# Performance work log

Measured on AMD Instinct MI355X. Metric: run time of the kernel, lower is better.

Reference implementation:

```python
import jax, jax.numpy as jnp
import numpy as np

B, S, D = 32, 4096, 64        # batch, n_vec, n_dim
L = 13                        # n_link_all (chord links: 0, 1, 2, 4, ..., 2048)
NW = 13                       # n_W sparse-multiply rounds
HF, HV = 128, 128             # fnet / vnet hidden widths
NC = 2                        # n_class
VOCAB = 512
OFFSETS = [0] + [2 ** k for k in range(L - 1)]  # static python ints


def setup_inputs() -> dict:
    key = jax.random.key(0)
    ks = jax.random.split(key, 8)
    sn = lambda k, shape, sc: (jax.random.normal(k, shape, jnp.float32) * sc)
    return {
        "inputs": jax.random.randint(ks[0], (B, S), 0, VOCAB),
        "emb":  sn(ks[1], (VOCAB, D), 1.0),          # frozen embedding table
        "fW1":  sn(ks[2], (NW, D, HF), 0.1),         # stacked FNet layer-1 weights
        "fb1":  jnp.zeros((NW, HF), jnp.float32),
        "fW2":  sn(ks[3], (NW, HF, L), 0.1),         # stacked FNet layer-2 weights
        "fb2":  jnp.zeros((NW, L), jnp.float32),
        "vW1":  sn(ks[4], (D, HV), 0.1),
        "vb1":  jnp.zeros((HV,), jnp.float32),
        "vW2":  sn(ks[5], (HV, D), 0.1),
        "vb2":  jnp.zeros((D,), jnp.float32),
        "finW": sn(ks[6], (NC, S * D), 0.02),        # torch Linear weight (out, in)
        "finb": jnp.zeros((NC,), jnp.float32),
    }


def _gelu(x):
    return jax.nn.gelu(x, approximate=False)  # torch nn.GELU default (erf)


def reference(inputs, emb, fW1, fb1, fW2, fb2, vW1, vb1, vW2, vb2, finW, finb):
    X = emb[inputs]                                                  # (B,S,D)
    # all NW FNets at once: (NW,B,S,L)
    H = _gelu(jnp.einsum('bsd,kdh->kbsh', X, fW1) + fb1[:, None, None, :])
    Fs = jnp.einsum('kbsh,khl->kbsl', H, fW2) + fb2[:, None, None, :]
    # VNet
    V = _gelu(X @ vW1 + vb1) @ vW2 + vb2                             # (B,S,D)
    # chord sparse multiply rounds with residual:
    # Z[b,i,:] <- sum_l F[b,i,l] * Z[b,(i+off_l) mod S,:]  ;  Z += V
    Z = V
    for k in range(NW):
        Fk = Fs[k]                                                   # (B,S,L)
        Zn = Fk[..., 0][..., None] * Z                               # offset 0
        for l in range(1, L):
            Zn = Zn + Fk[..., l][..., None] * jnp.roll(Z, -OFFSETS[l], axis=1)
        Z = Zn + V
    # NOTE: original source computes logits from V (Z is overwritten); we
    # also return Z so the sparse-multiply loop stays live.
    out = V.reshape(B, S * D) @ finW.T + finb                        # (B,NC)
    return out, Z
```

## Files before the change

### kernel.cpp

```cpp
#include <hip/hip_runtime.h>
#include <hip/hip_bf16.h>
#include <hip/hip_fp16.h>
#include <math.h>

#define S_LEN   4096
#define B_SZ    32
#define D_DIM   64
#define L_LNK   13
#define NW_R    13
#define HF_W    128
#define HV_W    128
#define VOCAB_N 512
#define NC_N    2

#define STRIDE  512
#define NROW    8
#define MIRROR  256
#define BUFN    (S_LEN + MIRROR)

typedef float vf4 __attribute__((ext_vector_type(4)));

__device__ __forceinline__ float gelu_erf(float x) {
    return 0.5f * x * (1.0f + erff(x * 0.70710678118654752440f));
}

__device__ __forceinline__ uint2 pack4h(vf4 v) {
    __half2 a = __float22half2_rn(float2{v.x, v.y});
    __half2 b = __float22half2_rn(float2{v.z, v.w});
    uint2 r;
    r.x = *reinterpret_cast<unsigned int*>(&a);
    r.y = *reinterpret_cast<unsigned int*>(&b);
    return r;
}

__device__ __forceinline__ void fma_mix4_lo(vf4& a, unsigned cw, uint2 z) {
    float x = a.x, y = a.y, zz = a.z, w = a.w;
    asm("v_fma_mix_f32 %0, %4, %5, %0 op_sel:[0,0,0] op_sel_hi:[1,1,0]\n\t"
        "v_fma_mix_f32 %1, %4, %5, %1 op_sel:[0,1,0] op_sel_hi:[1,1,0]\n\t"
        "v_fma_mix_f32 %2, %4, %6, %2 op_sel:[0,0,0] op_sel_hi:[1,1,0]\n\t"
        "v_fma_mix_f32 %3, %4, %6, %3 op_sel:[0,1,0] op_sel_hi:[1,1,0]"
        : "+v"(x), "+v"(y), "+v"(zz), "+v"(w)
        : "v"(cw), "v"(z.x), "v"(z.y));
    a.x = x; a.y = y; a.z = zz; a.w = w;
}

__device__ __forceinline__ void fma_mix4_hi(vf4& a, unsigned cw, uint2 z) {
    float x = a.x, y = a.y, zz = a.z, w = a.w;
    asm("v_fma_mix_f32 %0, %4, %5, %0 op_sel:[1,0,0] op_sel_hi:[1,1,0]\n\t"
        "v_fma_mix_f32 %1, %4, %5, %1 op_sel:[1,1,0] op_sel_hi:[1,1,0]\n\t"
        "v_fma_mix_f32 %2, %4, %6, %2 op_sel:[1,0,0] op_sel_hi:[1,1,0]\n\t"
        "v_fma_mix_f32 %3, %4, %6, %3 op_sel:[1,1,0] op_sel_hi:[1,1,0]"
        : "+v"(x), "+v"(y), "+v"(zz), "+v"(w)
        : "v"(cw), "v"(z.x), "v"(z.y));
    a.x = x; a.y = y; a.z = zz; a.w = w;
}

__device__ __forceinline__ vf4 fma_mix4_init(unsigned cw, uint2 z, vf4 c) {
    float x, y, zz, w;
    asm("v_fma_mix_f32 %0, %4, %5, %7 op_sel:[0,0,0] op_sel_hi:[1,1,0]\n\t"
        "v_fma_mix_f32 %1, %4, %5, %8 op_sel:[0,1,0] op_sel_hi:[1,1,0]\n\t"
        "v_fma_mix_f32 %2, %4, %6, %9 op_sel:[0,0,0] op_sel_hi:[1,1,0]\n\t"
        "v_fma_mix_f32 %3, %4, %6, %10 op_sel:[0,1,0] op_sel_hi:[1,1,0]"
        : "=&v"(x), "=&v"(y), "=&v"(zz), "=&v"(w)
        : "v"(cw), "v"(z.x), "v"(z.y),
          "v"(c.x), "v"(c.y), "v"(c.z), "v"(c.w));
    vf4 r; r.x = x; r.y = y; r.z = zz; r.w = w;
    return r;
}

__global__ __launch_bounds__(128)
void tables_kernel(const float* __restrict__ emb,
                   const float* __restrict__ fW1, const float* __restrict__ fb1,
                   const float* __restrict__ fW2, const float* __restrict__ fb2,
                   const float* __restrict__ vW1, const float* __restrict__ vb1,
                   const float* __restrict__ vW2, const float* __restrict__ vb2,
                   __half* __restrict__ F_table, float* __restrict__ V_table) {
    __shared__ float s_emb[D_DIM];
    __shared__ float s_H[HF_W];
    const int blk = blockIdx.x;
    const int tid = threadIdx.x;

    if (blk < NW_R * VOCAB_N) {
        const int k = blk >> 9;
        const int t = blk & (VOCAB_N - 1);
        if (tid < D_DIM) s_emb[tid] = emb[t * D_DIM + tid];
        __syncthreads();
        float acc = fb1[k * HF_W + tid];
        const float* w = fW1 + (size_t)k * D_DIM * HF_W + tid;
        #pragma unroll 8
        for (int d = 0; d < D_DIM; ++d) acc += s_emb[d] * w[d * HF_W];
        s_H[tid] = gelu_erf(acc);
        __syncthreads();
        if (tid < 16) {
            float o = 0.0f;
            if (tid < L_LNK) {
                o = fb2[k * L_LNK + tid];
                const float* w2 = fW2 + (size_t)k * HF_W * L_LNK + tid;
                #pragma unroll 8
                for (int h = 0; h < HF_W; ++h) o += s_H[h] * w2[h * L_LNK];
            }
            F_table[((size_t)(k * VOCAB_N + t)) * 16 + tid] = __float2half_rn(o);
        }
    } else {
        const int t = blk - NW_R * VOCAB_N;
        if (tid < D_DIM) s_emb[tid] = emb[t * D_DIM + tid];
        __syncthreads();
        float acc = vb1[tid];
        const float* w = vW1 + tid;
        #pragma unroll 8
        for (int d = 0; d < D_DIM; ++d) acc += s_emb[d] * w[d * HV_W];
        s_H[tid] = gelu_erf(acc);
        __syncthreads();
        if (tid < D_DIM) {
            float o = vb2[tid];
            const float* w2 = vW2 + tid;
            #pragma unroll 8
            for (int h = 0; h < HV_W; ++h) o += s_H[h] * w2[h * D_DIM];
            V_table[t * D_DIM + tid] = o;
        }
    }
}

__global__ __launch_bounds__(512)
void logits_kernel(const int* __restrict__ tok,
                   const float* __restrict__ V_table,
                   const float* __restrict__ finW,
                   const float* __restrict__ finb,
                   float* __restrict__ out) {
    const int b = blockIdx.x >> 3;
    const int chunk = blockIdx.x & 7;
    const int tid = threadIdx.x;
    const int s = chunk * 512 + tid;
    const int t = tok[b * S_LEN + s];
    const float4* vp = (const float4*)V_table + t * 16;
    const float4* f0 = (const float4*)finW + s * 16;
    const float4* f1 = (const float4*)(finW + (size_t)S_LEN * D_DIM) + s * 16;
    float a0 = 0.0f, a1 = 0.0f;
    #pragma unroll
    for (int j = 0; j < 16; ++j) {
        float4 v = vp[j], x = f0[j], y = f1[j];
        a0 += v.x * x.x + v.y * x.y + v.z * x.z + v.w * x.w;
        a1 += v.x * y.x + v.y * y.y + v.z * y.z + v.w * y.w;
    }
    #pragma unroll
    for (int o = 32; o > 0; o >>= 1) {
        a0 += __shfl_down(a0, o, 64);
        a1 += __shfl_down(a1, o, 64);
    }
    __shared__ float sp[2][8];
    if ((tid & 63) == 0) { sp[0][tid >> 6] = a0; sp[1][tid >> 6] = a1; }
    __syncthreads();
    if (tid == 0) {
        float s0 = 0.0f, s1 = 0.0f;
        #pragma unroll
        for (int i = 0; i < 8; ++i) { s0 += sp[0][i]; s1 += sp[1][i]; }
        if (chunk == 0) { s0 += finb[0]; s1 += finb[1]; }
        atomicAdd(&out[b * NC_N + 0], s0);
        atomicAdd(&out[b * NC_N + 1], s1);
    }
}

__global__ __launch_bounds__(512, 4)
void chord_kernel(const int* __restrict__ tok,
                  const __half* __restrict__ F_table,
                  const float* __restrict__ V_table,
                  float* __restrict__ Zout) {
    __shared__ uint2 Zs[2][BUFN];
    const int b = blockIdx.y;
    const int ds = blockIdx.x;
    const int t = threadIdx.x;
    const vf4* V4 = (const vf4*)V_table;

    unsigned tokf[NROW];
    vf4 Vf[NROW];
    uint2 zp[NROW];
    #pragma unroll
    for (int j = 0; j < NROW; ++j) {
        const int r = t + STRIDE * j;
        const int tk = tok[b * S_LEN + r];
        tokf[j] = (unsigned)tk * 32u;
        vf4 v = V4[tk * 16 + ds];
        Vf[j] = v;
        uint2 p = pack4h(v);
        zp[j] = p;
        Zs[0][r] = p;
    }
    if (t < MIRROR) Zs[0][S_LEN + t] = zp[0];
    __syncthreads();

    int cur = 0;
    vf4 acc[NROW];
    #pragma unroll 1
    for (int k = 0; k < NW_R; ++k) {
        const char* Fk = (const char*)F_table + (size_t)k * (VOCAB_N * 32);
        const uint2* Zc = Zs[cur];
        #pragma unroll
        for (int j = 0; j < NROW; ++j) {
            const int r = t + STRIDE * j;
            const char* Fr = Fk + tokf[j];
            uint4 u0 = *(const uint4*)Fr;
            uint2 u1 = *(const uint2*)(Fr + 16);
            unsigned u2 = *(const unsigned*)(Fr + 24);
            vf4 a = fma_mix4_init(u0.x, zp[j], Vf[j]);
            fma_mix4_lo(a, u1.y, zp[(j + 1) & 7]);
            fma_mix4_hi(a, u1.y, zp[(j + 2) & 7]);
            fma_mix4_lo(a, u2,   zp[(j + 4) & 7]);
            fma_mix4_hi(a, u0.x, Zc[r + 1]);
            fma_mix4_lo(a, u0.y, Zc[r + 2]);
            fma_mix4_hi(a, u0.y, Zc[r + 4]);
            fma_mix4_lo(a, u0.z, Zc[r + 8]);
            fma_mix4_hi(a, u0.z, Zc[r + 16]);
            fma_mix4_lo(a, u0.w, Zc[r + 32]);
            fma_mix4_hi(a, u0.w, Zc[r + 64]);
            fma_mix4_lo(a, u1.x, Zc[r + 128]);
            fma_mix4_hi(a, u1.x, Zc[r + 256]);
            acc[j] = a;
        }
        if (k < NW_R - 1) {
            uint2* Zn = Zs[cur ^ 1];
            #pragma unroll
            for (int j = 0; j < NROW; ++j) {
                uint2 p = pack4h(acc[j]);
                zp[j] = p;
                Zn[t + STRIDE * j] = p;
            }
            if (t < MIRROR) Zn[S_LEN + t] = zp[0];
        }
        __syncthreads();
        cur ^= 1;
    }

    #pragma unroll
    for (int j = 0; j < NROW; ++j) {
        const int r = t + STRIDE * j;
        *(vf4*)(Zout + (((size_t)b * S_LEN + r) << 6) + ds * 4) = acc[j];
    }
}

extern "C" void kernel_launch(void* const* d_in, const int* in_sizes, int n_in,
                              void* d_out, int out_size, void* d_ws, size_t ws_size,
                              hipStream_t stream) {
    const int*   tok  = (const int*)d_in[0];
    const float* emb  = (const float*)d_in[1];
    const float* fW1  = (const float*)d_in[2];
    const float* fb1  = (const float*)d_in[3];
    const float* fW2  = (const float*)d_in[4];
    const float* fb2  = (const float*)d_in[5];
    const float* vW1  = (const float*)d_in[6];
    const float* vb1  = (const float*)d_in[7];
    const float* vW2  = (const float*)d_in[8];
    const float* vb2  = (const float*)d_in[9];
    const float* finW = (const float*)d_in[10];
    const float* finb = (const float*)d_in[11];

    float* out = (float*)d_out;
    float* Z   = out + B_SZ * NC_N;

    float*  V_table = (float*)d_ws;
    __half* F_table = (__half*)(V_table + VOCAB_N * D_DIM);

    hipMemsetAsync(out, 0, B_SZ * NC_N * sizeof(float), stream);
    tables_kernel<<<NW_R * VOCAB_N + VOCAB_N, 128, 0, stream>>>(
        emb, fW1, fb1, fW2, fb2, vW1, vb1, vW2, vb2, F_table, V_table);
    logits_kernel<<<B_SZ * NC_N * 4, 512, 0, stream>>>(tok, V_table, finW, finb, out);
    chord_kernel<<<dim3(16, B_SZ), 512, 0, stream>>>(tok, F_table, V_table, Z);
}
```

Before: 215.7 us.

## Double chord block size, keep V in half, parallelize FNet layer-2 reduction

The chord kernel now uses 1024 threads with 4 rows each instead of 512 threads with 8 rows. The offset-512 link moves from registers to shared memory, and the mirror region grows to 512 entries. V is kept as packed halves and fed as the addend of the initial mixed FMA, which cuts register pressure and is meant to raise latency hiding. In the tables kernel, the serial 13-thread layer-2 dot product becomes a per-thread partial product reduced by wave shuffles. The costs are one extra LDS read per row, V rounded to fp16 inside the accumulation, and a larger shared buffer.

```diff
diff --git a/kernel.cpp b/kernel.cpp
--- a/kernel.cpp
+++ b/kernel.cpp
@@ -13,9 +13,10 @@
 #define VOCAB_N 512
 #define NC_N    2
 
-#define STRIDE  512
-#define NROW    8
-#define MIRROR  256
+#define NT      1024
+#define STRIDE  1024
+#define NROW    4
+#define MIRROR  512
 #define BUFN    (S_LEN + MIRROR)
 
 typedef float vf4 __attribute__((ext_vector_type(4)));
@@ -55,15 +56,14 @@
     a.x = x; a.y = y; a.z = zz; a.w = w;
 }
 
-__device__ __forceinline__ vf4 fma_mix4_init(unsigned cw, uint2 z, vf4 c) {
+__device__ __forceinline__ vf4 fma_mix4_init_h(unsigned cw, uint2 z, uint2 v) {
     float x, y, zz, w;
-    asm("v_fma_mix_f32 %0, %4, %5, %7 op_sel:[0,0,0] op_sel_hi:[1,1,0]\n\t"
-        "v_fma_mix_f32 %1, %4, %5, %8 op_sel:[0,1,0] op_sel_hi:[1,1,0]\n\t"
-        "v_fma_mix_f32 %2, %4, %6, %9 op_sel:[0,0,0] op_sel_hi:[1,1,0]\n\t"
-        "v_fma_mix_f32 %3, %4, %6, %10 op_sel:[0,1,0] op_sel_hi:[1,1,0]"
+    asm("v_fma_mix_f32 %0, %4, %5, %7 op_sel:[0,0,0] op_sel_hi:[1,1,1]\n\t"
+        "v_fma_mix_f32 %1, %4, %5, %7 op_sel:[0,1,1] op_sel_hi:[1,1,1]\n\t"
+        "v_fma_mix_f32 %2, %4, %6, %8 op_sel:[0,0,0] op_sel_hi:[1,1,1]\n\t"
+        "v_fma_mix_f32 %3, %4, %6, %8 op_sel:[0,1,1] op_sel_hi:[1,1,1]"
         : "=&v"(x), "=&v"(y), "=&v"(zz), "=&v"(w)
-        : "v"(cw), "v"(z.x), "v"(z.y),
-          "v"(c.x), "v"(c.y), "v"(c.z), "v"(c.w));
+        : "v"(cw), "v"(z.x), "v"(z.y), "v"(v.x), "v"(v.y));
     vf4 r; r.x = x; r.y = y; r.z = zz; r.w = w;
     return r;
 }
@@ -77,6 +77,7 @@
                    __half* __restrict__ F_table, float* __restrict__ V_table) {
     __shared__ float s_emb[D_DIM];
     __shared__ float s_H[HF_W];
+    __shared__ float s_red[2][16];
     const int blk = blockIdx.x;
     const int tid = threadIdx.x;
 
@@ -89,16 +90,24 @@
         const float* w = fW1 + (size_t)k * D_DIM * HF_W + tid;
         #pragma unroll 8
         for (int d = 0; d < D_DIM; ++d) acc += s_emb[d] * w[d * HF_W];
-        s_H[tid] = gelu_erf(acc);
-        __syncthreads();
-        if (tid < 16) {
-            float o = 0.0f;
-            if (tid < L_LNK) {
-                o = fb2[k * L_LNK + tid];
-                const float* w2 = fW2 + (size_t)k * HF_W * L_LNK + tid;
-                #pragma unroll 8
-                for (int h = 0; h < HF_W; ++h) o += s_H[h] * w2[h * L_LNK];
-            }
+        const float hval = gelu_erf(acc);
+        const float* w2 = fW2 + ((size_t)k * HF_W + tid) * L_LNK;
+        float p[L_LNK];
+        #pragma unroll
+        for (int l = 0; l < L_LNK; ++l) p[l] = hval * w2[l];
+        #pragma unroll
+        for (int o = 1; o < 64; o <<= 1) {
+            #pragma unroll
+            for (int l = 0; l < L_LNK; ++l) p[l] += __shfl_xor(p[l], o, 64);
+        }
+        if ((tid & 63) == 0) {
+            const int wv = tid >> 6;
+            #pragma unroll
+            for (int l = 0; l < L_LNK; ++l) s_red[wv][l] = p[l];
+        }
+        __syncthreads();
+        if (tid < L_LNK) {
+            float o = fb2[k * L_LNK + tid] + s_red[0][tid] + s_red[1][tid];
             F_table[((size_t)(k * VOCAB_N + t)) * 16 + tid] = __float2half_rn(o);
         }
     } else {
@@ -160,7 +169,7 @@
     }
 }
 
-__global__ __launch_bounds__(512, 4)
+__global__ __launch_bounds__(NT, 8)
 void chord_kernel(const int* __restrict__ tok,
                   const __half* __restrict__ F_table,
                   const float* __restrict__ V_table,
@@ -172,17 +181,14 @@
     const vf4* V4 = (const vf4*)V_table;
 
     unsigned tokf[NROW];
-    vf4 Vf[NROW];
-    uint2 zp[NROW];
+    uint2 Vp[NROW], zp[NROW];
     #pragma unroll
     for (int j = 0; j < NROW; ++j) {
         const int r = t + STRIDE * j;
         const int tk = tok[b * S_LEN + r];
         tokf[j] = (unsigned)tk * 32u;
-        vf4 v = V4[tk * 16 + ds];
-        Vf[j] = v;
-        uint2 p = pack4h(v);
-        zp[j] = p;
+        uint2 p = pack4h(V4[tk * 16 + ds]);
+        Vp[j] = p; zp[j] = p;
         Zs[0][r] = p;
     }
     if (t < MIRROR) Zs[0][S_LEN + t] = zp[0];
@@ -201,10 +207,9 @@
             uint4 u0 = *(const uint4*)Fr;
             uint2 u1 = *(const uint2*)(Fr + 16);
             unsigned u2 = *(const unsigned*)(Fr + 24);
-            vf4 a = fma_mix4_init(u0.x, zp[j], Vf[j]);
-            fma_mix4_lo(a, u1.y, zp[(j + 1) & 7]);
-            fma_mix4_hi(a, u1.y, zp[(j + 2) & 7]);
-            fma_mix4_lo(a, u2,   zp[(j + 4) & 7]);
+            vf4 a = fma_mix4_init_h(u0.x, zp[j], Vp[j]);
+            fma_mix4_hi(a, u1.y, zp[(j + 1) & 3]);
+            fma_mix4_lo(a, u2,   zp[(j + 2) & 3]);
             fma_mix4_hi(a, u0.x, Zc[r + 1]);
             fma_mix4_lo(a, u0.y, Zc[r + 2]);
             fma_mix4_hi(a, u0.y, Zc[r + 4]);
@@ -214,6 +219,7 @@
             fma_mix4_hi(a, u0.w, Zc[r + 64]);
             fma_mix4_lo(a, u1.x, Zc[r + 128]);
             fma_mix4_hi(a, u1.x, Zc[r + 256]);
+            fma_mix4_lo(a, u1.y, Zc[r + 512]);
             acc[j] = a;
         }
         if (k < NW_R - 1) {
@@ -263,5 +269,5 @@
     tables_kernel<<<NW_R * VOCAB_N + VOCAB_N, 128, 0, stream>>>(
         emb, fW1, fb1, fW2, fb2, vW1, vb1, vW2, vb2, F_table, V_table);
     logits_kernel<<<B_SZ * NC_N * 4, 512, 0, stream>>>(tok, V_table, finW, finb, out);
-    chord_kernel<<<dim3(16, B_SZ), 512, 0, stream>>>(tok, F_table, V_table, Z);
-}
+    chord_kernel<<<dim3(16, B_SZ), NT, 0, stream>>>(tok, F_table, V_table, Z);
+}
```

Result: no change. 215.1 us (-0.3%).
